# Optimization experiments

Hardware: AMD Instinct MI355X
Metric: run time of the kernel (lower is better)

Reference implementation:

```python
import jax, jax.numpy as jnp
import numpy as np
from functools import partial

T_DEC, T_ENC = 64, 256
B, E, D = 32, 256, 512   # batch, audio_encoder_size(=input_size), decoder_hidden_size
N_MEL = 80               # spectral_size == n_mel_channels


def setup_inputs() -> dict:
    key = jax.random.key(0)
    ks = jax.random.split(key, 9)
    s = 0.02
    return {
        "decoder_inputs": jax.random.normal(ks[0], (T_DEC, B, E), jnp.float32),
        "alignment_inputs": jax.random.normal(ks[1], (T_ENC, B, E), jnp.float32),
        "W_att": jax.random.normal(ks[2], (E, D), jnp.float32) * s,      # LinearNorm(D->E, no bias)
        "W_ih": jax.random.normal(ks[3], (3 * D, 2 * E), jnp.float32) * s,  # GRUCell input weights (r,z,n)
        "W_hh": jax.random.normal(ks[4], (3 * D, D), jnp.float32) * s,      # GRUCell hidden weights
        "W_mel": jax.random.normal(ks[5], (N_MEL, D + E), jnp.float32) * s,
        "b_mel": jax.random.normal(ks[6], (N_MEL,), jnp.float32) * s,
        "W_gate": jax.random.normal(ks[7], (1, D + E), jnp.float32) * s,
        "b_gate": jax.random.normal(ks[8], (1,), jnp.float32) * s,
    }


def _decode_loop(decoder_inputs, alignment_inputs, W_att, W_ih, W_hh, W_mel, b_mel, W_gate, b_gate):
    Bd, Dd = decoder_inputs.shape[1], W_hh.shape[1]

    def step(h, dec_in):
        # --- Attention: per-feature softmax over encoder time, collapsed over features ---
        proj = h @ W_att.T                                  # (B, E)
        scores = alignment_inputs * proj[None]              # (T_enc, B, E)
        w = jax.nn.softmax(scores, axis=0)                  # softmax over encoder time
        tw = w.sum(axis=-1)                                 # (T_enc, B): sum of per-feature weights
        ctx = jnp.einsum('tb,tbe->be', tw, alignment_inputs)  # (B, E)
        # --- GRUCell (bias=False) ---
        x = jnp.concatenate([dec_in, ctx], axis=-1)         # (B, 2E)
        gi = x @ W_ih.T                                     # (B, 3D)
        gh = h @ W_hh.T                                     # (B, 3D)
        ir, iz, inn = jnp.split(gi, 3, axis=-1)
        hr, hz, hn = jnp.split(gh, 3, axis=-1)
        r = jax.nn.sigmoid(ir + hr)
        z = jax.nn.sigmoid(iz + hz)
        n = jnp.tanh(inn + r * hn)
        h_new = (1.0 - z) * n + z * h
        h_new = jax.nn.relu(h_new)                          # relu(dropout(h)), dropout=0
        # --- Output heads ---
        dhac = jnp.concatenate([ctx, h_new], axis=-1)       # (B, E+D)
        mel = dhac @ W_mel.T + b_mel                        # (B, N_MEL)
        gate = dhac @ W_gate.T + b_gate                     # (B, 1)
        return h_new, (mel, gate)

    # prepend zero init frame, drop last frame (teacher forcing, T_dec steps)
    init_frame = jnp.zeros((1,) + decoder_inputs.shape[1:], decoder_inputs.dtype)
    seq = jnp.concatenate([init_frame, decoder_inputs[:-1]], axis=0)
    h0 = jnp.zeros((Bd, Dd), decoder_inputs.dtype)
    _, (mels, gates) = jax.lax.scan(step, h0, seq)
    # parse_decoder_outputs
    n_mel = W_mel.shape[0]
    mel_out = mels.transpose(1, 0, 2).reshape(Bd, -1, n_mel).transpose(0, 2, 1)  # (B, n_mel, T_dec)
    gate_out = gates.transpose(1, 0, 2)                                          # (B, T_dec, 1)
    return mel_out, gate_out


def reference(decoder_inputs, alignment_inputs, W_att, W_ih, W_hh, W_mel, b_mel, W_gate, b_gate):
    return _decode_loop(decoder_inputs, alignment_inputs, W_att, W_ih, W_hh,
                        W_mel, b_mel, W_gate, b_gate)
```

## Files before the change

### kernel.cpp

```cpp
#include <hip/hip_runtime.h>
#include <hip/hip_bf16.h>


#define LOG2E 1.4426950408889634f
#define FLAGS_MAGIC 0x13572468u
#define SMEM_BYTES 138752
#define NBLK 162

typedef __attribute__((ext_vector_type(8))) short bf8;
typedef __attribute__((ext_vector_type(4))) float f32x4;
typedef __attribute__((ext_vector_type(4))) unsigned u32x4;
typedef unsigned long long ull;

#define EX2(x) exp2f(x)
#define MFMA16(a, b, c) __builtin_amdgcn_mfma_f32_16x16x32_bf16(a, b, c, 0, 0, 0)

struct Params {
  const float* dec;
  const float* ali;
  const float* watt;
  const float* wih;
  const float* whh;
  const float* wmel;
  const float* bmel;
  const float* wgate;
  const float* bgate;
  float* out;
  unsigned* bar;
  __hip_bfloat16* wihb;
  __hip_bfloat16* whhb;
  __hip_bfloat16* wmelgb;
  __hip_bfloat16* seqb;
  __hip_bfloat16* hbf;
  __hip_bfloat16* ctxb;
  unsigned* wattp;
};

__device__ __forceinline__ bf8 ldfrag(const __hip_bfloat16* p) { return *(const bf8*)p; }
__device__ __forceinline__ float sigm(float x) { return 1.0f / (1.0f + EX2(-x * LOG2E)); }
__device__ __forceinline__ float tanhfast(float x) {
  x = fminf(fmaxf(x, -15.0f), 15.0f);
  float e = EX2(x * (2.0f * LOG2E));
  return (e - 1.0f) / (e + 1.0f);
}
__device__ __forceinline__ float btof(unsigned v) { return __uint_as_float(v << 16); }
__device__ __forceinline__ unsigned short f2bfbits(float x) {
  __hip_bfloat16 h = __float2bfloat16(x);
  return *(unsigned short*)&h;
}
__device__ __forceinline__ unsigned sysld32(const unsigned* p) {
  return __hip_atomic_load(p, __ATOMIC_RELAXED, __HIP_MEMORY_SCOPE_SYSTEM);
}
__device__ __forceinline__ ull sysld64(const ull* p) {
  return __hip_atomic_load(p, __ATOMIC_RELAXED, __HIP_MEMORY_SCOPE_SYSTEM);
}
__device__ __forceinline__ void sysst32(unsigned* p, unsigned v) {
  __hip_atomic_store(p, v, __ATOMIC_RELAXED, __HIP_MEMORY_SCOPE_SYSTEM);
}
__device__ __forceinline__ void sysst64(ull* p, ull v) {
  __hip_atomic_store(p, v, __ATOMIC_RELAXED, __HIP_MEMORY_SCOPE_SYSTEM);
}
__device__ __forceinline__ void sysld16x4(u32x4* d0, u32x4* d1, u32x4* d2, u32x4* d3,
                                          const void* p0, const void* p1,
                                          const void* p2, const void* p3) {
  u32x4 a, b, c, d;
  asm volatile(
      "global_load_dwordx4 %0, %4, off sc0 sc1\n\t"
      "global_load_dwordx4 %1, %5, off sc0 sc1\n\t"
      "global_load_dwordx4 %2, %6, off sc0 sc1\n\t"
      "global_load_dwordx4 %3, %7, off sc0 sc1\n\t"
      "s_waitcnt vmcnt(0)"
      : "=&v"(a), "=&v"(b), "=&v"(c), "=&v"(d)
      : "v"(p0), "v"(p1), "v"(p2), "v"(p3)
      : "memory");
  *d0 = a; *d1 = b; *d2 = c; *d3 = d;
}
__device__ __forceinline__ void sysld16x8(u32x4* d0, u32x4* d1, u32x4* d2, u32x4* d3,
                                          u32x4* d4, u32x4* d5, u32x4* d6, u32x4* d7,
                                          const void* p0, const void* p1,
                                          const void* p2, const void* p3,
                                          const void* p4, const void* p5,
                                          const void* p6, const void* p7) {
  u32x4 a, b, c, d, e, f, g, h;
  asm volatile(
      "global_load_dwordx4 %0, %8, off sc0 sc1\n\t"
      "global_load_dwordx4 %1, %9, off sc0 sc1\n\t"
      "global_load_dwordx4 %2, %10, off sc0 sc1\n\t"
      "global_load_dwordx4 %3, %11, off sc0 sc1\n\t"
      "global_load_dwordx4 %4, %12, off sc0 sc1\n\t"
      "global_load_dwordx4 %5, %13, off sc0 sc1\n\t"
      "global_load_dwordx4 %6, %14, off sc0 sc1\n\t"
      "global_load_dwordx4 %7, %15, off sc0 sc1\n\t"
      "s_waitcnt vmcnt(0)"
      : "=&v"(a), "=&v"(b), "=&v"(c), "=&v"(d),
        "=&v"(e), "=&v"(f), "=&v"(g), "=&v"(h)
      : "v"(p0), "v"(p1), "v"(p2), "v"(p3),
        "v"(p4), "v"(p5), "v"(p6), "v"(p7)
      : "memory");
  *d0 = a; *d1 = b; *d2 = c; *d3 = d;
  *d4 = e; *d5 = f; *d6 = g; *d7 = h;
}
__device__ __forceinline__ void waitge(unsigned* w, unsigned tgt) {
  while (sysld32(w) < tgt) __builtin_amdgcn_s_sleep(1);
}

__device__ __forceinline__ void p0bar(unsigned* bar) {
  __syncthreads();
  if (threadIdx.x == 0) {
    __builtin_amdgcn_fence(__ATOMIC_RELEASE, "agent");
    __hip_atomic_fetch_add(bar + 16, 1u, __ATOMIC_RELAXED, __HIP_MEMORY_SCOPE_SYSTEM);
    while (sysld32(bar + 16) < (unsigned)NBLK) __builtin_amdgcn_s_sleep(1);
    __builtin_amdgcn_fence(__ATOMIC_ACQUIRE, "agent");
  }
  __syncthreads();
}

__device__ __forceinline__ void p0a_worker(const Params& p, int wid) {
  for (int i = wid; i < 2252800; i += 17408) {
    if (i < 786432) {
      p.wihb[i] = __float2bfloat16(p.wih[i]);
    } else if (i < 1572864) {
      int j = i - 786432;
      p.whhb[j] = __float2bfloat16(p.whh[j]);
    } else if (i < 2097152) {
      int j = i - 1572864;
      int s = j >> 13;
      p.seqb[j] = (s == 0) ? __float2bfloat16(0.0f) : __float2bfloat16(p.dec[j - 8192]);
    } else if (i < 2170880) {
      int j = i - 2097152;
      int r = j / 768, c = j - r * 768;
      float v = (r < 80) ? p.wmel[j] : ((r == 80) ? p.wgate[c] : 0.0f);
      p.wmelgb[j] = __float2bfloat16(v);
    } else if (i < 2236416) {
      int j = i - 2170880;
      int kp = j >> 8, e = j & 255;
      unsigned lo = f2bfbits(p.watt[e * 512 + 2 * kp]);
      unsigned hi = f2bfbits(p.watt[e * 512 + 2 * kp + 1]);
      p.wattp[j] = lo | (hi << 16);
    } else {
      int j = i - 2236416;
      p.hbf[j] = __float2bfloat16(0.0f);
    }
  }
}

__device__ __forceinline__ void stage_h_frag(__hip_bfloat16* hA,
                                             const __hip_bfloat16* hsrc, int tid) {
  const int lm = tid & 15, lq = (tid >> 4) & 3, wq = tid >> 6;
  const int dst_in = (lq * 16 + lm) * 8;
  const int i0 = wq, i1 = 8 + wq, i2 = 16 + wq, i3 = 24 + wq;
  auto soff = [&](int idx) {
    return ((idx >> 4) * 16 + lm) * 512 + (idx & 15) * 32 + lq * 8;
  };
  u32x4 a, b, c, d;
  sysld16x4(&a, &b, &c, &d, hsrc + soff(i0), hsrc + soff(i1), hsrc + soff(i2),
            hsrc + soff(i3));
  u32x4* dst = (u32x4*)hA;
  dst[(i0 * 512 + dst_in) >> 3] = a;
  dst[(i1 * 512 + dst_in) >> 3] = b;
  dst[(i2 * 512 + dst_in) >> 3] = c;
  dst[(i3 * 512 + dst_in) >> 3] = d;
}
__device__ __forceinline__ void stage_c4(__hip_bfloat16* cA,
                                         const __hip_bfloat16* csrc, int tid) {
  const int lm = tid & 15, lq = (tid >> 4) & 3, wq = tid >> 6;
  const int dst_in = (lq * 16 + lm) * 8;
  u32x4* dst = (u32x4*)cA;
  auto soff = [&](int idx) {
    int mt = idx >> 5, kt = idx & 31;
    int bb = mt * 16 + lm;
    int k = kt * 32 + lq * 8;
    return ((k >> 8) * 32 + bb) * 256 + (k & 255);
  };
  const int i0 = wq, i1 = 8 + wq, i2 = 16 + wq, i3 = 24 + wq;
  const int i4 = 32 + wq, i5 = 40 + wq, i6 = 48 + wq, i7 = 56 + wq;
  u32x4 a, b, c, d, e, f, g, h;
  sysld16x8(&a, &b, &c, &d, &e, &f, &g, &h,
            csrc + soff(i0), csrc + soff(i1), csrc + soff(i2), csrc + soff(i3),
            csrc + soff(i4), csrc + soff(i5), csrc + soff(i6), csrc + soff(i7));
  dst[(i0 * 512 + dst_in) >> 3] = a;
  dst[(i1 * 512 + dst_in) >> 3] = b;
  dst[(i2 * 512 + dst_in) >> 3] = c;
  dst[(i3 * 512 + dst_in) >> 3] = d;
  dst[(i4 * 512 + dst_in) >> 3] = e;
  dst[(i5 * 512 + dst_in) >> 3] = f;
  dst[(i6 * 512 + dst_in) >> 3] = g;
  dst[(i7 * 512 + dst_in) >> 3] = h;
}

__global__ void __launch_bounds__(512, 1) rdec_kernel(Params p) {
  const int tid = threadIdx.x;
  const int bid = blockIdx.x;
  extern __shared__ char smem[];
  unsigned* hdone = p.bar + 32;
  unsigned* ctxdone = p.bar + 544;
  unsigned* meldone = p.bar + 2592;

  if (bid == 0) {
    for (int i = 1 + tid; i < 2624; i += 512) sysst32(p.bar + i, 0u);
    __syncthreads();
    if (tid == 0) sysst32(p.bar, FLAGS_MAGIC);
  }

  if (bid < 128) {
    const int b = bid >> 2, q4 = bid & 3, hb = q4 * 32 + b;
    unsigned short* alds = (unsigned short*)smem;
    float* fb = (float*)(smem + 133120);
    float* shh = fb;
    float* p2l = fb + 512;
    float* rzl = fb + 576;
    float* tw = fb + 640;
    float* cp = fb + 896;

    const int el = (tid & 7) | ((tid >> 6) << 3);
    const int kq = (tid >> 3) & 7;
    const int f = tid & 255, th = tid >> 8;

    for (int i = tid; i < 65536; i += 512) {
      int t = i >> 8, ee = i & 255;
      alds[ee * 260 + t] = f2bfbits(p.ali[t * 8192 + b * 256 + ee]);
    }
    if (tid == 0) {
      while (sysld32(p.bar) != FLAGS_MAGIC) __builtin_amdgcn_s_sleep(1);
    }
    p0bar(p.bar);
    unsigned wr[32];
#pragma unroll
    for (int i = 0; i < 32; ++i) wr[i] = p.wattp[(i * 8 + kq) * 256 + q4 * 64 + el];

    for (int s = 0; s < 64; ++s) {
      if (tid < 32) waitge(hdone + tid * 16, (unsigned)s);
      else if (tid < 34) waitge(meldone + (tid - 32) * 16, (s >= 4) ? (unsigned)(s - 3) : 0u);
      __syncthreads();
      if (tid < 128) {
        ull w = sysld64((const ull*)(p.hbf + (s & 3) * 16384 + b * 512) + tid);
        shh[tid * 4 + 0] = btof((unsigned)(w & 0xffff));
        shh[tid * 4 + 1] = btof((unsigned)((w >> 16) & 0xffff));
        shh[tid * 4 + 2] = btof((unsigned)((w >> 32) & 0xffff));
        shh[tid * 4 + 3] = btof((unsigned)((w >> 48) & 0xffff));
      }
      __syncthreads();
      {
        const float2* h2 = (const float2*)shh;
        float a0 = 0.f, a1 = 0.f;
#pragma unroll
        for (int i = 0; i < 32; i += 2) {
          unsigned w0 = wr[i], w1 = wr[i + 1];
          float2 h0 = h2[i * 8 + kq], h1 = h2[(i + 1) * 8 + kq];
          a0 = fmaf(__uint_as_float(w0 << 16), h0.x, a0);
          a0 = fmaf(__uint_as_float(w0 & 0xffff0000u), h0.y, a0);
          a1 = fmaf(__uint_as_float(w1 << 16), h1.x, a1);
          a1 = fmaf(__uint_as_float(w1 & 0xffff0000u), h1.y, a1);
        }
        float pr = a0 + a1;
        pr += __shfl_xor(pr, 8);
        pr += __shfl_xor(pr, 16);
        pr += __shfl_xor(pr, 32);
        const float pp = pr * LOG2E;
        const unsigned short* ap = alds + (q4 * 64 + el) * 260 + kq * 32;
        float z0 = 0.f, z1 = 0.f;
#pragma unroll
        for (int j = 0; j < 8; ++j) {
          ushort4 v = *(const ushort4*)(ap + j * 4);
          z0 += EX2(btof(v.x) * pp) + EX2(btof(v.y) * pp);
          z1 += EX2(btof(v.z) * pp) + EX2(btof(v.w) * pp);
        }
        float zz = z0 + z1;
        zz += __shfl_xor(zz, 8);
        zz += __shfl_xor(zz, 16);
        zz += __shfl_xor(zz, 32);
        if (kq == 0) {
          p2l[el] = pp;
          rzl[el] = 1.0f / zz;
        }
      }
      __syncthreads();
      {
        float t0 = 0.f, t1 = 0.f, t2 = 0.f, t3 = 0.f;
#pragma unroll
        for (int j = 0; j < 8; ++j) {
          const int e2 = kq * 8 + j;
          ushort4 v = *(const ushort4*)(alds + (q4 * 64 + e2) * 260 + el * 4);
          const float ppj = p2l[e2], rr = rzl[e2];
          t0 = fmaf(EX2(btof(v.x) * ppj), rr, t0);
          t1 = fmaf(EX2(btof(v.y) * ppj), rr, t1);
          t2 = fmaf(EX2(btof(v.z) * ppj), rr, t2);
          t3 = fmaf(EX2(btof(v.w) * ppj), rr, t3);
        }
        t0 += __shfl_xor(t0, 8); t0 += __shfl_xor(t0, 16); t0 += __shfl_xor(t0, 32);
        t1 += __shfl_xor(t1, 8); t1 += __shfl_xor(t1, 16); t1 += __shfl_xor(t1, 32);
        t2 += __shfl_xor(t2, 8); t2 += __shfl_xor(t2, 16); t2 += __shfl_xor(t2, 32);
        t3 += __shfl_xor(t3, 8); t3 += __shfl_xor(t3, 16); t3 += __shfl_xor(t3, 32);
        if (kq == 0) *(float4*)(tw + el * 4) = make_float4(t0, t1, t2, t3);
      }
      __syncthreads();
      {
        const unsigned short* ap = alds + f * 260 + th * 128;
        const float4* twv = (const float4*)(tw + th * 128);
        float c0 = 0.f, c1 = 0.f;
#pragma unroll 4
        for (int j = 0; j < 32; ++j) {
          ushort4 v = *(const ushort4*)(ap + j * 4);
          float4 t4 = twv[j];
          c0 += t4.x * btof(v.x) + t4.y * btof(v.y);
          c1 += t4.z * btof(v.z) + t4.w * btof(v.w);
        }
        cp[th * 256 + f] = c0 + c1;
      }
      __syncthreads();
      if (tid < 128) {
        float2 ca = ((const float2*)cp)[tid];
        float2 cb = ((const float2*)(cp + 256))[tid];
        float cv0 = ca.x + cb.x, cv1 = ca.y + cb.y;
        unsigned u = (unsigned)f2bfbits(cv0) | ((unsigned)f2bfbits(cv1) << 16);
        sysst32((unsigned*)(p.ctxb + ((s & 3) * 128 + hb) * 256) + tid, u);
      }
      __syncthreads();
      if (tid == 0) sysst32(ctxdone + hb * 16, (unsigned)(s + 1));
    }
  } else if (bid < 160) {
    const int dt = bid - 128;
    const int wv = tid >> 6;
    const bool act = wv < 6;
    const int l = tid & 63, lm = l & 15, lq = l >> 4;
    const int g = wv % 3, mt = wv / 3;
    const int am = mt * 16 + lm;
    const int brow = g * 512 + dt * 16 + lm;
    __hip_bfloat16* hA = (__hip_bfloat16*)smem;
    __hip_bfloat16* cA = (__hip_bfloat16*)(smem + 32768);
    float* pw = (float*)(smem + 98304);
    unsigned short* h16 = (unsigned short*)(smem + 107008);
    p0a_worker(p, (bid - 128) * 512 + tid);
    if (tid == 0) {
      while (sysld32(p.bar) != FLAGS_MAGIC) __builtin_amdgcn_s_sleep(1);
    }
    p0bar(p.bar);
    bf8 WH[16], WD[8], WC[8];
    if (act) {
#pragma unroll
      for (int kt = 0; kt < 16; ++kt) WH[kt] = ldfrag(p.whhb + brow * 512 + kt * 32 + lq * 8);
#pragma unroll
      for (int kt = 0; kt < 8; ++kt) WD[kt] = ldfrag(p.wihb + brow * 512 + kt * 32 + lq * 8);
#pragma unroll
      for (int kt = 0; kt < 8; ++kt) WC[kt] = ldfrag(p.wihb + brow * 512 + 256 + kt * 32 + lq * 8);
    }
    for (int s = 0; s < 64; ++s) {
      if (tid < 32) waitge(hdone + tid * 16, (unsigned)s);
      else if (tid < 34) waitge(meldone + (tid - 32) * 16, (s >= 4) ? (unsigned)(s - 3) : 0u);
      __syncthreads();
      stage_h_frag(hA, p.hbf + (s & 3) * 16384, tid);
      __syncthreads();
      f32x4 acc = {0.f, 0.f, 0.f, 0.f};
      f32x4 gi = {0.f, 0.f, 0.f, 0.f};
      if (act) {
#pragma unroll
        for (int kt = 0; kt < 16; ++kt) {
          bf8 a = ldfrag(hA + (mt * 16 + kt) * 512 + l * 8);
          acc = MFMA16(a, WH[kt], acc);
        }
        const __hip_bfloat16* seqp = p.seqb + s * 8192;
#pragma unroll
        for (int kt = 0; kt < 8; ++kt) {
          bf8 a = ldfrag(seqp + am * 256 + kt * 32 + lq * 8);
          gi = MFMA16(a, WD[kt], gi);
        }
      }
      if (tid < 128) waitge(ctxdone + tid * 16, (unsigned)(s + 1));
      __syncthreads();
      stage_c4(cA, p.ctxb + (s & 3) * 32768, tid);
      __syncthreads();
      if (act) {
#pragma unroll
        for (int kt = 0; kt < 32; ++kt) {
          bf8 a = ldfrag(cA + (mt * 32 + kt) * 512 + l * 8);
          gi = MFMA16(a, WC[kt & 7], gi);
        }
        if (g < 2) {
#pragma unroll
          for (int r = 0; r < 4; ++r) pw[(wv * 16 + lq * 4 + r) * 17 + lm] = acc[r] + gi[r];
        } else {
#pragma unroll
          for (int r = 0; r < 4; ++r) pw[(wv * 16 + lq * 4 + r) * 17 + lm] = acc[r];
#pragma unroll
          for (int r = 0; r < 4; ++r) pw[((6 + mt) * 16 + lq * 4 + r) * 17 + lm] = gi[r];
        }
      }
      __syncthreads();
      {
        const int bb = tid >> 4, dl = tid & 15;
        const int mtb = bb >> 4, bl = bb & 15;
        float rg = sigm(pw[((mtb * 3 + 0) * 16 + bl) * 17 + dl]);
        float zg = sigm(pw[((mtb * 3 + 1) * 16 + bl) * 17 + dl]);
        float hn = pw[((mtb * 3 + 2) * 16 + bl) * 17 + dl];
        float inn = pw[((6 + mtb) * 16 + bl) * 17 + dl];
        float nn = tanhfast(fmaf(rg, hn, inn));
        const int d = dt * 16 + dl;
        float ho = btof(((unsigned short*)hA)[((bb >> 4) * 16 + (d >> 5)) * 512 +
                                              (((d >> 3) & 3) * 16 + (bb & 15)) * 8 +
                                              (d & 7)]);
        float hnew = fmaxf(0.0f, fmaf(zg, ho - nn, nn));
        h16[bb * 16 + dl] = f2bfbits(hnew);
      }
      __syncthreads();
      if (tid < 256) {
        const int bb2 = tid >> 3, dp = tid & 7;
        unsigned v = (unsigned)h16[bb2 * 16 + dp * 2] |
                     ((unsigned)h16[bb2 * 16 + dp * 2 + 1] << 16);
        sysst32((unsigned*)(p.hbf + ((s + 1) & 3) * 16384) + bb2 * 256 + dt * 8 + dp, v);
      }
      __syncthreads();
      if (tid == 0) sysst32(hdone + dt * 16, (unsigned)(s + 1));
    }
  } else {
    const int mt = bid - 160;
    const int wv = tid >> 6;
    const bool act = wv < 6;
    const int l = tid & 63, lm = l & 15, lq = l >> 4;
    const int nt = wv;
    const int bn = nt * 16 + lm;
    __hip_bfloat16* hA = (__hip_bfloat16*)smem;
    __hip_bfloat16* cA = (__hip_bfloat16*)(smem + 32768);
    p0a_worker(p, (bid - 128) * 512 + tid);
    if (tid == 0) {
      while (sysld32(p.bar) != FLAGS_MAGIC) __builtin_amdgcn_s_sleep(1);
    }
    p0bar(p.bar);
    bf8 WMC[8], WMH[16];
    float bias = 0.f;
    if (act) {
#pragma unroll
      for (int kt = 0; kt < 8; ++kt) WMC[kt] = ldfrag(p.wmelgb + bn * 768 + kt * 32 + lq * 8);
#pragma unroll
      for (int kt = 0; kt < 16; ++kt)
        WMH[kt] = ldfrag(p.wmelgb + bn * 768 + 256 + kt * 32 + lq * 8);
      bias = (bn < 80) ? p.bmel[bn] : ((bn == 80) ? p.bgate[0] : 0.f);
    }
    for (int tau = 0; tau < 64; ++tau) {
      if (tid < 32) waitge(hdone + tid * 16, (unsigned)(tau + 1));
      else if (tid >= 64 && tid < 192) waitge(ctxdone + (tid - 64) * 16, (unsigned)(tau + 1));
      __syncthreads();
      stage_h_frag(hA, p.hbf + ((tau + 1) & 3) * 16384, tid);
      stage_c4(cA, p.ctxb + (tau & 3) * 32768, tid);
      __syncthreads();
      if (act) {
        f32x4 acc = {0.f, 0.f, 0.f, 0.f};
#pragma unroll
        for (int kt = 0; kt < 48; ++kt) {
          bf8 a = (kt < 32) ? ldfrag(cA + (mt * 32 + kt) * 512 + l * 8)
                            : ldfrag(hA + (mt * 16 + (kt - 32)) * 512 + l * 8);
          bf8 bb2 = (kt < 32) ? WMC[kt & 7] : WMH[kt - 32];
          acc = MFMA16(a, bb2, acc);
        }
#pragma unroll
        for (int r = 0; r < 4; ++r) {
          int bb = mt * 16 + lq * 4 + r;
          float v = acc[r] + bias;
          if (bn < 80)
            p.out[bb * 5120 + bn * 64 + tau] = v;
          else if (bn == 80)
            p.out[163840 + bb * 64 + tau] = v;
        }
      }
      __syncthreads();
      if (tid == 0) sysst32(meldone + mt * 16, (unsigned)(tau + 1));
    }
  }
}

extern "C" void kernel_launch(void* const* d_in, const int* in_sizes, int n_in,
                              void* d_out, int out_size, void* d_ws, size_t ws_size,
                              hipStream_t stream) {
  Params P;
  P.dec = (const float*)d_in[0];
  P.ali = (const float*)d_in[1];
  P.watt = (const float*)d_in[2];
  P.wih = (const float*)d_in[3];
  P.whh = (const float*)d_in[4];
  P.wmel = (const float*)d_in[5];
  P.bmel = (const float*)d_in[6];
  P.wgate = (const float*)d_in[7];
  P.bgate = (const float*)d_in[8];
  P.out = (float*)d_out;

  char* w = (char*)d_ws;
  size_t o = 0;
  auto nxt = [&](size_t b) {
    char* r = w + o;
    o += (b + 255) & ~(size_t)255;
    return r;
  };
  P.bar = (unsigned*)nxt(16384);
  P.wihb = (__hip_bfloat16*)nxt(1536 * 512 * 2);
  P.whhb = (__hip_bfloat16*)nxt(1536 * 512 * 2);
  P.wmelgb = (__hip_bfloat16*)nxt(96 * 768 * 2);
  P.seqb = (__hip_bfloat16*)nxt(64 * 32 * 256 * 2);
  P.hbf = (__hip_bfloat16*)nxt(4 * 32 * 512 * 2);
  P.ctxb = (__hip_bfloat16*)nxt(4 * 128 * 256 * 2);
  P.wattp = (unsigned*)nxt(256 * 256 * 4);

  (void)hipFuncSetAttribute((const void*)rdec_kernel,
                            hipFuncAttributeMaxDynamicSharedMemorySize, SMEM_BYTES);

  void* args[] = {&P};
  hipError_t err = hipLaunchCooperativeKernel((void*)rdec_kernel, dim3(NBLK), dim3(512),
                                              args, SMEM_BYTES, stream);
  if (err != hipSuccess) {
    rdec_kernel<<<dim3(NBLK), dim3(512), SMEM_BYTES, stream>>>(P);
  }
}
```

Measured before the change: 822.6 us.

## Fold mel/gate head into GRU blocks and compute context via MFMA

Drops the two dedicated mel/gate blocks and runs the output-head MFMAs on idle waves of the first six GRU blocks, reusing the h and ctx tiles those blocks already stage in shared memory. This removes the meldone back-pressure waits and the extra grid-barrier participants. The attention context reduction becomes an MFMA, with the softmax weights split into high and low bf16 halves to keep precision. The encoder LDS row stride is padded to 264, and the spin-wait loses its sleep so it polls more aggressively, which raises memory-system traffic while blocks wait.

```diff
diff --git a/kernel.cpp b/kernel.cpp
--- a/kernel.cpp
+++ b/kernel.cpp
@@ -4,8 +4,8 @@
 
 #define LOG2E 1.4426950408889634f
 #define FLAGS_MAGIC 0x13572468u
-#define SMEM_BYTES 138752
-#define NBLK 162
+#define SMEM_BYTES 139776
+#define NBLK 160
 
 typedef __attribute__((ext_vector_type(8))) short bf8;
 typedef __attribute__((ext_vector_type(4))) float f32x4;
@@ -101,7 +101,7 @@
   *d4 = e; *d5 = f; *d6 = g; *d7 = h;
 }
 __device__ __forceinline__ void waitge(unsigned* w, unsigned tgt) {
-  while (sysld32(w) < tgt) __builtin_amdgcn_s_sleep(1);
+  while (sysld32(w) < tgt) {}
 }
 
 __device__ __forceinline__ void p0bar(unsigned* bar) {
@@ -116,7 +116,7 @@
 }
 
 __device__ __forceinline__ void p0a_worker(const Params& p, int wid) {
-  for (int i = wid; i < 2252800; i += 17408) {
+  for (int i = wid; i < 2252800; i += 16384) {
     if (i < 786432) {
       p.wihb[i] = __float2bfloat16(p.wih[i]);
     } else if (i < 1572864) {
@@ -194,7 +194,6 @@
   extern __shared__ char smem[];
   unsigned* hdone = p.bar + 32;
   unsigned* ctxdone = p.bar + 544;
-  unsigned* meldone = p.bar + 2592;
 
   if (bid == 0) {
     for (int i = 1 + tid; i < 2624; i += 512) sysst32(p.bar + i, 0u);
@@ -205,20 +204,21 @@
   if (bid < 128) {
     const int b = bid >> 2, q4 = bid & 3, hb = q4 * 32 + b;
     unsigned short* alds = (unsigned short*)smem;
-    float* fb = (float*)(smem + 133120);
+    float* fb = (float*)(smem + 135168);
     float* shh = fb;
     float* p2l = fb + 512;
     float* rzl = fb + 576;
-    float* tw = fb + 640;
-    float* cp = fb + 896;
+    float* ctxf = fb + 640;
+    unsigned short* twb = (unsigned short*)(fb + 896);
 
     const int el = (tid & 7) | ((tid >> 6) << 3);
     const int kq = (tid >> 3) & 7;
-    const int f = tid & 255, th = tid >> 8;
+    const int w = tid >> 6, l = tid & 63;
+    const int lm = l & 15, lq = l >> 4;
 
     for (int i = tid; i < 65536; i += 512) {
       int t = i >> 8, ee = i & 255;
-      alds[ee * 260 + t] = f2bfbits(p.ali[t * 8192 + b * 256 + ee]);
+      alds[ee * 264 + t] = f2bfbits(p.ali[t * 8192 + b * 256 + ee]);
     }
     if (tid == 0) {
       while (sysld32(p.bar) != FLAGS_MAGIC) __builtin_amdgcn_s_sleep(1);
@@ -230,14 +230,13 @@
 
     for (int s = 0; s < 64; ++s) {
       if (tid < 32) waitge(hdone + tid * 16, (unsigned)s);
-      else if (tid < 34) waitge(meldone + (tid - 32) * 16, (s >= 4) ? (unsigned)(s - 3) : 0u);
       __syncthreads();
       if (tid < 128) {
-        ull w = sysld64((const ull*)(p.hbf + (s & 3) * 16384 + b * 512) + tid);
-        shh[tid * 4 + 0] = btof((unsigned)(w & 0xffff));
-        shh[tid * 4 + 1] = btof((unsigned)((w >> 16) & 0xffff));
-        shh[tid * 4 + 2] = btof((unsigned)((w >> 32) & 0xffff));
-        shh[tid * 4 + 3] = btof((unsigned)((w >> 48) & 0xffff));
+        ull wv = sysld64((const ull*)(p.hbf + (s & 3) * 16384 + b * 512) + tid);
+        shh[tid * 4 + 0] = btof((unsigned)(wv & 0xffff));
+        shh[tid * 4 + 1] = btof((unsigned)((wv >> 16) & 0xffff));
+        shh[tid * 4 + 2] = btof((unsigned)((wv >> 32) & 0xffff));
+        shh[tid * 4 + 3] = btof((unsigned)((wv >> 48) & 0xffff));
       }
       __syncthreads();
       {
@@ -257,7 +256,7 @@
         pr += __shfl_xor(pr, 16);
         pr += __shfl_xor(pr, 32);
         const float pp = pr * LOG2E;
-        const unsigned short* ap = alds + (q4 * 64 + el) * 260 + kq * 32;
+        const unsigned short* ap = alds + (q4 * 64 + el) * 264 + kq * 32;
         float z0 = 0.f, z1 = 0.f;
 #pragma unroll
         for (int j = 0; j < 8; ++j) {
@@ -280,7 +279,7 @@
 #pragma unroll
         for (int j = 0; j < 8; ++j) {
           const int e2 = kq * 8 + j;
-          ushort4 v = *(const ushort4*)(alds + (q4 * 64 + e2) * 260 + el * 4);
+          ushort4 v = *(const ushort4*)(alds + (q4 * 64 + e2) * 264 + el * 4);
           const float ppj = p2l[e2], rr = rzl[e2];
           t0 = fmaf(EX2(btof(v.x) * ppj), rr, t0);
           t1 = fmaf(EX2(btof(v.y) * ppj), rr, t1);
@@ -291,34 +290,49 @@
         t1 += __shfl_xor(t1, 8); t1 += __shfl_xor(t1, 16); t1 += __shfl_xor(t1, 32);
         t2 += __shfl_xor(t2, 8); t2 += __shfl_xor(t2, 16); t2 += __shfl_xor(t2, 32);
         t3 += __shfl_xor(t3, 8); t3 += __shfl_xor(t3, 16); t3 += __shfl_xor(t3, 32);
-        if (kq == 0) *(float4*)(tw + el * 4) = make_float4(t0, t1, t2, t3);
+        if (kq == 0) {
+          unsigned short h0 = f2bfbits(t0), h1 = f2bfbits(t1);
+          unsigned short h2c = f2bfbits(t2), h3 = f2bfbits(t3);
+          unsigned short l0 = f2bfbits(t0 - btof(h0)), l1 = f2bfbits(t1 - btof(h1));
+          unsigned short l2 = f2bfbits(t2 - btof(h2c)), l3 = f2bfbits(t3 - btof(h3));
+          *(ull*)(twb + el * 4) =
+              (ull)h0 | ((ull)h1 << 16) | ((ull)h2c << 32) | ((ull)h3 << 48);
+          *(ull*)(twb + 256 + el * 4) =
+              (ull)l0 | ((ull)l1 << 16) | ((ull)l2 << 32) | ((ull)l3 << 48);
+        }
       }
       __syncthreads();
       {
-        const unsigned short* ap = alds + f * 260 + th * 128;
-        const float4* twv = (const float4*)(tw + th * 128);
-        float c0 = 0.f, c1 = 0.f;
-#pragma unroll 4
-        for (int j = 0; j < 32; ++j) {
-          ushort4 v = *(const ushort4*)(ap + j * 4);
-          float4 t4 = twv[j];
-          c0 += t4.x * btof(v.x) + t4.y * btof(v.y);
-          c1 += t4.z * btof(v.z) + t4.w * btof(v.w);
-        }
-        cp[th * 256 + f] = c0 + c1;
+        bf8 tb[16];
+#pragma unroll
+        for (int kt = 0; kt < 16; ++kt)
+          tb[kt] = *(const bf8*)(twb + (kt >> 3) * 256 + (kt & 7) * 32 + lq * 8);
+#pragma unroll
+        for (int half = 0; half < 2; ++half) {
+          const int mt = w * 2 + half;
+          bf8 af[8];
+#pragma unroll
+          for (int kt = 0; kt < 8; ++kt)
+            af[kt] = *(const bf8*)(alds + (mt * 16 + lm) * 264 + kt * 32 + lq * 8);
+          f32x4 acc = {0.f, 0.f, 0.f, 0.f};
+#pragma unroll
+          for (int kt = 0; kt < 16; ++kt) acc = MFMA16(af[kt & 7], tb[kt], acc);
+          if (lm == 0) {
+#pragma unroll
+            for (int r = 0; r < 4; ++r) ctxf[mt * 16 + lq * 4 + r] = acc[r];
+          }
+        }
       }
       __syncthreads();
       if (tid < 128) {
-        float2 ca = ((const float2*)cp)[tid];
-        float2 cb = ((const float2*)(cp + 256))[tid];
-        float cv0 = ca.x + cb.x, cv1 = ca.y + cb.y;
+        float cv0 = ctxf[2 * tid], cv1 = ctxf[2 * tid + 1];
         unsigned u = (unsigned)f2bfbits(cv0) | ((unsigned)f2bfbits(cv1) << 16);
         sysst32((unsigned*)(p.ctxb + ((s & 3) * 128 + hb) * 256) + tid, u);
       }
       __syncthreads();
       if (tid == 0) sysst32(ctxdone + hb * 16, (unsigned)(s + 1));
     }
-  } else if (bid < 160) {
+  } else {
     const int dt = bid - 128;
     const int wv = tid >> 6;
     const bool act = wv < 6;
@@ -344,9 +358,22 @@
 #pragma unroll
       for (int kt = 0; kt < 8; ++kt) WC[kt] = ldfrag(p.wihb + brow * 512 + 256 + kt * 32 + lq * 8);
     }
+    const bool melw = (dt < 6) && (wv >= 6);
+    bf8 WMC[8], WMH[16];
+    float mbias = 0.f;
+    int mmt = 0, bn = 0;
+    if (melw) {
+      mmt = wv - 6;
+      bn = dt * 16 + lm;
+#pragma unroll
+      for (int kt = 0; kt < 8; ++kt) WMC[kt] = ldfrag(p.wmelgb + bn * 768 + kt * 32 + lq * 8);
+#pragma unroll
+      for (int kt = 0; kt < 16; ++kt)
+        WMH[kt] = ldfrag(p.wmelgb + bn * 768 + 256 + kt * 32 + lq * 8);
+      mbias = (bn < 80) ? p.bmel[bn] : ((bn == 80) ? p.bgate[0] : 0.f);
+    }
     for (int s = 0; s < 64; ++s) {
       if (tid < 32) waitge(hdone + tid * 16, (unsigned)s);
-      else if (tid < 34) waitge(meldone + (tid - 32) * 16, (s >= 4) ? (unsigned)(s - 3) : 0u);
       __syncthreads();
       stage_h_frag(hA, p.hbf + (s & 3) * 16384, tid);
       __syncthreads();
@@ -363,6 +390,25 @@
         for (int kt = 0; kt < 8; ++kt) {
           bf8 a = ldfrag(seqp + am * 256 + kt * 32 + lq * 8);
           gi = MFMA16(a, WD[kt], gi);
+        }
+      } else if (melw && s > 0) {
+        const int tau = s - 1;
+        f32x4 macc = {0.f, 0.f, 0.f, 0.f};
+#pragma unroll
+        for (int kt = 0; kt < 48; ++kt) {
+          bf8 a = (kt < 32) ? ldfrag(cA + (mmt * 32 + kt) * 512 + l * 8)
+                            : ldfrag(hA + (mmt * 16 + (kt - 32)) * 512 + l * 8);
+          bf8 bb2 = (kt < 32) ? WMC[kt & 7] : WMH[kt - 32];
+          macc = MFMA16(a, bb2, macc);
+        }
+#pragma unroll
+        for (int r = 0; r < 4; ++r) {
+          int bb = mmt * 16 + lq * 4 + r;
+          float v = macc[r] + mbias;
+          if (bn < 80)
+            p.out[bb * 5120 + bn * 64 + tau] = v;
+          else if (bn == 80)
+            p.out[163840 + bb * 64 + tau] = v;
         }
       }
       if (tid < 128) waitge(ctxdone + tid * 16, (unsigned)(s + 1));
@@ -411,58 +457,30 @@
       __syncthreads();
       if (tid == 0) sysst32(hdone + dt * 16, (unsigned)(s + 1));
     }
-  } else {
-    const int mt = bid - 160;
-    const int wv = tid >> 6;
-    const bool act = wv < 6;
-    const int l = tid & 63, lm = l & 15, lq = l >> 4;
-    const int nt = wv;
-    const int bn = nt * 16 + lm;
-    __hip_bfloat16* hA = (__hip_bfloat16*)smem;
-    __hip_bfloat16* cA = (__hip_bfloat16*)(smem + 32768);
-    p0a_worker(p, (bid - 128) * 512 + tid);
-    if (tid == 0) {
-      while (sysld32(p.bar) != FLAGS_MAGIC) __builtin_amdgcn_s_sleep(1);
-    }
-    p0bar(p.bar);
-    bf8 WMC[8], WMH[16];
-    float bias = 0.f;
-    if (act) {
-#pragma unroll
-      for (int kt = 0; kt < 8; ++kt) WMC[kt] = ldfrag(p.wmelgb + bn * 768 + kt * 32 + lq * 8);
-#pragma unroll
-      for (int kt = 0; kt < 16; ++kt)
-        WMH[kt] = ldfrag(p.wmelgb + bn * 768 + 256 + kt * 32 + lq * 8);
-      bias = (bn < 80) ? p.bmel[bn] : ((bn == 80) ? p.bgate[0] : 0.f);
-    }
-    for (int tau = 0; tau < 64; ++tau) {
-      if (tid < 32) waitge(hdone + tid * 16, (unsigned)(tau + 1));
-      else if (tid >= 64 && tid < 192) waitge(ctxdone + (tid - 64) * 16, (unsigned)(tau + 1));
-      __syncthreads();
-      stage_h_frag(hA, p.hbf + ((tau + 1) & 3) * 16384, tid);
-      stage_c4(cA, p.ctxb + (tau & 3) * 32768, tid);
-      __syncthreads();
-      if (act) {
-        f32x4 acc = {0.f, 0.f, 0.f, 0.f};
+    if (dt < 6) {
+      if (tid < 32) waitge(hdone + tid * 16, 64u);
+      __syncthreads();
+      stage_h_frag(hA, p.hbf + 0, tid);
+      __syncthreads();
+      if (melw) {
+        f32x4 macc = {0.f, 0.f, 0.f, 0.f};
 #pragma unroll
         for (int kt = 0; kt < 48; ++kt) {
-          bf8 a = (kt < 32) ? ldfrag(cA + (mt * 32 + kt) * 512 + l * 8)
-                            : ldfrag(hA + (mt * 16 + (kt - 32)) * 512 + l * 8);
+          bf8 a = (kt < 32) ? ldfrag(cA + (mmt * 32 + kt) * 512 + l * 8)
+                            : ldfrag(hA + (mmt * 16 + (kt - 32)) * 512 + l * 8);
           bf8 bb2 = (kt < 32) ? WMC[kt & 7] : WMH[kt - 32];
-          acc = MFMA16(a, bb2, acc);
+          macc = MFMA16(a, bb2, macc);
         }
 #pragma unroll
         for (int r = 0; r < 4; ++r) {
-          int bb = mt * 16 + lq * 4 + r;
-          float v = acc[r] + bias;
+          int bb = mmt * 16 + lq * 4 + r;
+          float v = macc[r] + mbias;
           if (bn < 80)
-            p.out[bb * 5120 + bn * 64 + tau] = v;
+            p.out[bb * 5120 + bn * 64 + 63] = v;
           else if (bn == 80)
-            p.out[163840 + bb * 64 + tau] = v;
-        }
-      }
-      __syncthreads();
-      if (tid == 0) sysst32(meldone + mt * 16, (unsigned)(tau + 1));
+            p.out[163840 + bb * 64 + 63] = v;
+        }
+      }
     }
   }
 }
```

New measurement: 856.6 us. +4.1%, slower.

## Publish ctx/h from one wavefront with drained stores, move flag polling to idle waves

Applied to the files above, without the earlier changes.

The ctx and h publication is narrowed to a single wavefront that issues wider system-scope stores, waits for them to drain, and then raises the done flag. This removes a block-wide __syncthreads between the data store and the flag store. The flag-polling lanes move to higher-numbered waves so they do not sit in the wavefront doing the stores or the MFMA work. Ordering now relies on the in-wave vmcnt drain instead of a block barrier, which is subtle for cross-block visibility, and the next iteration's barrier still serializes later work.

```diff
diff --git a/kernel.cpp b/kernel.cpp
--- a/kernel.cpp
+++ b/kernel.cpp
@@ -59,6 +59,14 @@
 }
 __device__ __forceinline__ void sysst64(ull* p, ull v) {
   __hip_atomic_store(p, v, __ATOMIC_RELAXED, __HIP_MEMORY_SCOPE_SYSTEM);
+}
+__device__ __forceinline__ void sysst8_drain(void* dst, ull v) {
+  asm volatile("global_store_dwordx2 %0, %1, off sc0 sc1\n\ts_waitcnt vmcnt(0)"
+               :: "v"(dst), "v"(v) : "memory");
+}
+__device__ __forceinline__ void sysst16_drain(void* dst, u32x4 v) {
+  asm volatile("global_store_dwordx4 %0, %1, off sc0 sc1\n\ts_waitcnt vmcnt(0)"
+               :: "v"(dst), "v"(v) : "memory");
 }
 __device__ __forceinline__ void sysld16x4(u32x4* d0, u32x4* d1, u32x4* d2, u32x4* d3,
                                           const void* p0, const void* p1,
@@ -229,8 +237,9 @@
     for (int i = 0; i < 32; ++i) wr[i] = p.wattp[(i * 8 + kq) * 256 + q4 * 64 + el];
 
     for (int s = 0; s < 64; ++s) {
-      if (tid < 32) waitge(hdone + tid * 16, (unsigned)s);
-      else if (tid < 34) waitge(meldone + (tid - 32) * 16, (s >= 4) ? (unsigned)(s - 3) : 0u);
+      if (tid >= 128 && tid < 160) waitge(hdone + (tid - 128) * 16, (unsigned)s);
+      else if (tid >= 160 && tid < 162)
+        waitge(meldone + (tid - 160) * 16, (s >= 4) ? (unsigned)(s - 3) : 0u);
       __syncthreads();
       if (tid < 128) {
         ull w = sysld64((const ull*)(p.hbf + (s & 3) * 16384 + b * 512) + tid);
@@ -308,15 +317,17 @@
         cp[th * 256 + f] = c0 + c1;
       }
       __syncthreads();
-      if (tid < 128) {
-        float2 ca = ((const float2*)cp)[tid];
-        float2 cb = ((const float2*)(cp + 256))[tid];
-        float cv0 = ca.x + cb.x, cv1 = ca.y + cb.y;
-        unsigned u = (unsigned)f2bfbits(cv0) | ((unsigned)f2bfbits(cv1) << 16);
-        sysst32((unsigned*)(p.ctxb + ((s & 3) * 128 + hb) * 256) + tid, u);
-      }
-      __syncthreads();
-      if (tid == 0) sysst32(ctxdone + hb * 16, (unsigned)(s + 1));
+      if (tid < 64) {
+        float4 ca = *(const float4*)(cp + 4 * tid);
+        float4 cb = *(const float4*)(cp + 256 + 4 * tid);
+        unsigned u0 = (unsigned)f2bfbits(ca.x + cb.x) |
+                      ((unsigned)f2bfbits(ca.y + cb.y) << 16);
+        unsigned u1 = (unsigned)f2bfbits(ca.z + cb.z) |
+                      ((unsigned)f2bfbits(ca.w + cb.w) << 16);
+        unsigned* dst = (unsigned*)(p.ctxb + ((s & 3) * 128 + hb) * 256) + 2 * tid;
+        sysst8_drain(dst, (ull)u0 | ((ull)u1 << 32));
+        if (tid == 0) sysst32(ctxdone + hb * 16, (unsigned)(s + 1));
+      }
     }
   } else if (bid < 160) {
     const int dt = bid - 128;
@@ -345,8 +356,9 @@
       for (int kt = 0; kt < 8; ++kt) WC[kt] = ldfrag(p.wihb + brow * 512 + 256 + kt * 32 + lq * 8);
     }
     for (int s = 0; s < 64; ++s) {
-      if (tid < 32) waitge(hdone + tid * 16, (unsigned)s);
-      else if (tid < 34) waitge(meldone + (tid - 32) * 16, (s >= 4) ? (unsigned)(s - 3) : 0u);
+      if (tid >= 384 && tid < 416) waitge(hdone + (tid - 384) * 16, (unsigned)s);
+      else if (tid >= 416 && tid < 418)
+        waitge(meldone + (tid - 416) * 16, (s >= 4) ? (unsigned)(s - 3) : 0u);
       __syncthreads();
       stage_h_frag(hA, p.hbf + (s & 3) * 16384, tid);
       __syncthreads();
@@ -365,7 +377,7 @@
           gi = MFMA16(a, WD[kt], gi);
         }
       }
-      if (tid < 128) waitge(ctxdone + tid * 16, (unsigned)(s + 1));
+      if (tid >= 384) waitge(ctxdone + (tid - 384) * 16, (unsigned)(s + 1));
       __syncthreads();
       stage_c4(cA, p.ctxb + (s & 3) * 32768, tid);
       __syncthreads();
@@ -402,14 +414,13 @@
         h16[bb * 16 + dl] = f2bfbits(hnew);
       }
       __syncthreads();
-      if (tid < 256) {
-        const int bb2 = tid >> 3, dp = tid & 7;
-        unsigned v = (unsigned)h16[bb2 * 16 + dp * 2] |
-                     ((unsigned)h16[bb2 * 16 + dp * 2 + 1] << 16);
-        sysst32((unsigned*)(p.hbf + ((s + 1) & 3) * 16384) + bb2 * 256 + dt * 8 + dp, v);
-      }
-      __syncthreads();
-      if (tid == 0) sysst32(hdone + dt * 16, (unsigned)(s + 1));
+      if (tid < 64) {
+        u32x4 hv = *(const u32x4*)(h16 + 8 * tid);
+        unsigned* dst = (unsigned*)(p.hbf + ((s + 1) & 3) * 16384) +
+                        (tid >> 1) * 256 + dt * 8 + (tid & 1) * 4;
+        sysst16_drain(dst, hv);
+        if (tid == 0) sysst32(hdone + dt * 16, (unsigned)(s + 1));
+      }
     }
   } else {
     const int mt = bid - 160;
```

Result: slower. 886.5 us (+7.8%).

## Replace flag-based step barriers with sentinel-polled, non-reused data buffers

Applied to the files above, without the earlier changes.

Removes the per-step done counters and waits. Consumers now poll the h and ctx data directly until no sentinel value remains. The ring buffers of depth 4 are replaced with fully unrolled buffers (65 steps for h, 64 for ctx) that are pre-filled with a sentinel, so producers never wait on consumers (the meldone back-pressure is gone). This cuts one flag round-trip and several __syncthreads per step, at the cost of more workspace memory and a sentinel fill at startup, plus a risk that the sentinel fill races with early producer writes or that a bf16 pair legitimately equals the sentinel.

```diff
diff --git a/kernel.cpp b/kernel.cpp
--- a/kernel.cpp
+++ b/kernel.cpp
@@ -4,6 +4,7 @@
 
 #define LOG2E 1.4426950408889634f
 #define FLAGS_MAGIC 0x13572468u
+#define SENT 0x7FFF7FFFu
 #define SMEM_BYTES 138752
 #define NBLK 162
 
@@ -55,9 +56,6 @@
   return __hip_atomic_load(p, __ATOMIC_RELAXED, __HIP_MEMORY_SCOPE_SYSTEM);
 }
 __device__ __forceinline__ void sysst32(unsigned* p, unsigned v) {
-  __hip_atomic_store(p, v, __ATOMIC_RELAXED, __HIP_MEMORY_SCOPE_SYSTEM);
-}
-__device__ __forceinline__ void sysst64(ull* p, ull v) {
   __hip_atomic_store(p, v, __ATOMIC_RELAXED, __HIP_MEMORY_SCOPE_SYSTEM);
 }
 __device__ __forceinline__ void sysld16x4(u32x4* d0, u32x4* d1, u32x4* d2, u32x4* d3,
@@ -100,8 +98,8 @@
   *d0 = a; *d1 = b; *d2 = c; *d3 = d;
   *d4 = e; *d5 = f; *d6 = g; *d7 = h;
 }
-__device__ __forceinline__ void waitge(unsigned* w, unsigned tgt) {
-  while (sysld32(w) < tgt) __builtin_amdgcn_s_sleep(1);
+__device__ __forceinline__ bool clean4(u32x4 v) {
+  return v[0] != SENT && v[1] != SENT && v[2] != SENT && v[3] != SENT;
 }
 
 __device__ __forceinline__ void p0bar(unsigned* bar) {
@@ -144,7 +142,7 @@
   }
 }
 
-__device__ __forceinline__ void stage_h_frag(__hip_bfloat16* hA,
+__device__ __forceinline__ void stage_h_poll(__hip_bfloat16* hA,
                                              const __hip_bfloat16* hsrc, int tid) {
   const int lm = tid & 15, lq = (tid >> 4) & 3, wq = tid >> 6;
   const int dst_in = (lq * 16 + lm) * 8;
@@ -153,16 +151,20 @@
     return ((idx >> 4) * 16 + lm) * 512 + (idx & 15) * 32 + lq * 8;
   };
   u32x4 a, b, c, d;
-  sysld16x4(&a, &b, &c, &d, hsrc + soff(i0), hsrc + soff(i1), hsrc + soff(i2),
-            hsrc + soff(i3));
+  for (;;) {
+    sysld16x4(&a, &b, &c, &d, hsrc + soff(i0), hsrc + soff(i1), hsrc + soff(i2),
+              hsrc + soff(i3));
+    if (clean4(a) && clean4(b) && clean4(c) && clean4(d)) break;
+    __builtin_amdgcn_s_sleep(1);
+  }
   u32x4* dst = (u32x4*)hA;
   dst[(i0 * 512 + dst_in) >> 3] = a;
   dst[(i1 * 512 + dst_in) >> 3] = b;
   dst[(i2 * 512 + dst_in) >> 3] = c;
   dst[(i3 * 512 + dst_in) >> 3] = d;
 }
-__device__ __forceinline__ void stage_c4(__hip_bfloat16* cA,
-                                         const __hip_bfloat16* csrc, int tid) {
+__device__ __forceinline__ void stage_c4_poll(__hip_bfloat16* cA,
+                                              const __hip_bfloat16* csrc, int tid) {
   const int lm = tid & 15, lq = (tid >> 4) & 3, wq = tid >> 6;
   const int dst_in = (lq * 16 + lm) * 8;
   u32x4* dst = (u32x4*)cA;
@@ -175,9 +177,14 @@
   const int i0 = wq, i1 = 8 + wq, i2 = 16 + wq, i3 = 24 + wq;
   const int i4 = 32 + wq, i5 = 40 + wq, i6 = 48 + wq, i7 = 56 + wq;
   u32x4 a, b, c, d, e, f, g, h;
-  sysld16x8(&a, &b, &c, &d, &e, &f, &g, &h,
-            csrc + soff(i0), csrc + soff(i1), csrc + soff(i2), csrc + soff(i3),
-            csrc + soff(i4), csrc + soff(i5), csrc + soff(i6), csrc + soff(i7));
+  for (;;) {
+    sysld16x8(&a, &b, &c, &d, &e, &f, &g, &h,
+              csrc + soff(i0), csrc + soff(i1), csrc + soff(i2), csrc + soff(i3),
+              csrc + soff(i4), csrc + soff(i5), csrc + soff(i6), csrc + soff(i7));
+    if (clean4(a) && clean4(b) && clean4(c) && clean4(d) &&
+        clean4(e) && clean4(f) && clean4(g) && clean4(h)) break;
+    __builtin_amdgcn_s_sleep(1);
+  }
   dst[(i0 * 512 + dst_in) >> 3] = a;
   dst[(i1 * 512 + dst_in) >> 3] = b;
   dst[(i2 * 512 + dst_in) >> 3] = c;
@@ -192,9 +199,6 @@
   const int tid = threadIdx.x;
   const int bid = blockIdx.x;
   extern __shared__ char smem[];
-  unsigned* hdone = p.bar + 32;
-  unsigned* ctxdone = p.bar + 544;
-  unsigned* meldone = p.bar + 2592;
 
   if (bid == 0) {
     for (int i = 1 + tid; i < 2624; i += 512) sysst32(p.bar + i, 0u);
@@ -216,6 +220,12 @@
     const int kq = (tid >> 3) & 7;
     const int f = tid & 255, th = tid >> 8;
 
+    {
+      unsigned* hb32 = (unsigned*)p.hbf;
+      unsigned* cb32 = (unsigned*)p.ctxb;
+      for (int i = bid * 512 + tid; i < 524288; i += 65536) hb32[8192 + i] = SENT;
+      for (int i = bid * 512 + tid; i < 1048576; i += 65536) cb32[i] = SENT;
+    }
     for (int i = tid; i < 65536; i += 512) {
       int t = i >> 8, ee = i & 255;
       alds[ee * 260 + t] = f2bfbits(p.ali[t * 8192 + b * 256 + ee]);
@@ -229,11 +239,14 @@
     for (int i = 0; i < 32; ++i) wr[i] = p.wattp[(i * 8 + kq) * 256 + q4 * 64 + el];
 
     for (int s = 0; s < 64; ++s) {
-      if (tid < 32) waitge(hdone + tid * 16, (unsigned)s);
-      else if (tid < 34) waitge(meldone + (tid - 32) * 16, (s >= 4) ? (unsigned)(s - 3) : 0u);
-      __syncthreads();
       if (tid < 128) {
-        ull w = sysld64((const ull*)(p.hbf + (s & 3) * 16384 + b * 512) + tid);
+        const ull* hsrc = (const ull*)(p.hbf + s * 16384 + b * 512) + tid;
+        ull w;
+        for (;;) {
+          w = sysld64(hsrc);
+          if ((unsigned)w != SENT && (unsigned)(w >> 32) != SENT) break;
+          __builtin_amdgcn_s_sleep(1);
+        }
         shh[tid * 4 + 0] = btof((unsigned)(w & 0xffff));
         shh[tid * 4 + 1] = btof((unsigned)((w >> 16) & 0xffff));
         shh[tid * 4 + 2] = btof((unsigned)((w >> 32) & 0xffff));
@@ -313,10 +326,9 @@
         float2 cb = ((const float2*)(cp + 256))[tid];
         float cv0 = ca.x + cb.x, cv1 = ca.y + cb.y;
         unsigned u = (unsigned)f2bfbits(cv0) | ((unsigned)f2bfbits(cv1) << 16);
-        sysst32((unsigned*)(p.ctxb + ((s & 3) * 128 + hb) * 256) + tid, u);
-      }
-      __syncthreads();
-      if (tid == 0) sysst32(ctxdone + hb * 16, (unsigned)(s + 1));
+        sysst32((unsigned*)(p.ctxb + (s * 128 + hb) * 256) + tid, u);
+      }
+      __syncthreads();
     }
   } else if (bid < 160) {
     const int dt = bid - 128;
@@ -345,10 +357,7 @@
       for (int kt = 0; kt < 8; ++kt) WC[kt] = ldfrag(p.wihb + brow * 512 + 256 + kt * 32 + lq * 8);
     }
     for (int s = 0; s < 64; ++s) {
-      if (tid < 32) waitge(hdone + tid * 16, (unsigned)s);
-      else if (tid < 34) waitge(meldone + (tid - 32) * 16, (s >= 4) ? (unsigned)(s - 3) : 0u);
-      __syncthreads();
-      stage_h_frag(hA, p.hbf + (s & 3) * 16384, tid);
+      stage_h_poll(hA, p.hbf + s * 16384, tid);
       __syncthreads();
       f32x4 acc = {0.f, 0.f, 0.f, 0.f};
       f32x4 gi = {0.f, 0.f, 0.f, 0.f};
@@ -365,9 +374,7 @@
           gi = MFMA16(a, WD[kt], gi);
         }
       }
-      if (tid < 128) waitge(ctxdone + tid * 16, (unsigned)(s + 1));
-      __syncthreads();
-      stage_c4(cA, p.ctxb + (s & 3) * 32768, tid);
+      stage_c4_poll(cA, p.ctxb + s * 32768, tid);
       __syncthreads();
       if (act) {
 #pragma unroll
@@ -406,10 +413,9 @@
         const int bb2 = tid >> 3, dp = tid & 7;
         unsigned v = (unsigned)h16[bb2 * 16 + dp * 2] |
                      ((unsigned)h16[bb2 * 16 + dp * 2 + 1] << 16);
-        sysst32((unsigned*)(p.hbf + ((s + 1) & 3) * 16384) + bb2 * 256 + dt * 8 + dp, v);
-      }
-      __syncthreads();
-      if (tid == 0) sysst32(hdone + dt * 16, (unsigned)(s + 1));
+        sysst32((unsigned*)(p.hbf + (s + 1) * 16384) + bb2 * 256 + dt * 8 + dp, v);
+      }
+      __syncthreads();
     }
   } else {
     const int mt = bid - 160;
@@ -436,11 +442,8 @@
       bias = (bn < 80) ? p.bmel[bn] : ((bn == 80) ? p.bgate[0] : 0.f);
     }
     for (int tau = 0; tau < 64; ++tau) {
-      if (tid < 32) waitge(hdone + tid * 16, (unsigned)(tau + 1));
-      else if (tid >= 64 && tid < 192) waitge(ctxdone + (tid - 64) * 16, (unsigned)(tau + 1));
-      __syncthreads();
-      stage_h_frag(hA, p.hbf + ((tau + 1) & 3) * 16384, tid);
-      stage_c4(cA, p.ctxb + (tau & 3) * 32768, tid);
+      stage_h_poll(hA, p.hbf + (tau + 1) * 16384, tid);
+      stage_c4_poll(cA, p.ctxb + tau * 32768, tid);
       __syncthreads();
       if (act) {
         f32x4 acc = {0.f, 0.f, 0.f, 0.f};
@@ -462,7 +465,6 @@
         }
       }
       __syncthreads();
-      if (tid == 0) sysst32(meldone + mt * 16, (unsigned)(tau + 1));
     }
   }
 }
@@ -494,8 +496,8 @@
   P.whhb = (__hip_bfloat16*)nxt(1536 * 512 * 2);
   P.wmelgb = (__hip_bfloat16*)nxt(96 * 768 * 2);
   P.seqb = (__hip_bfloat16*)nxt(64 * 32 * 256 * 2);
-  P.hbf = (__hip_bfloat16*)nxt(4 * 32 * 512 * 2);
-  P.ctxb = (__hip_bfloat16*)nxt(4 * 128 * 256 * 2);
+  P.hbf = (__hip_bfloat16*)nxt(65 * 32 * 512 * 2);
+  P.ctxb = (__hip_bfloat16*)nxt(64 * 128 * 256 * 2);
   P.wattp = (unsigned*)nxt(256 * 256 * 4);
 
   (void)hipFuncSetAttribute((const void*)rdec_kernel,
```

After: 822.5 us. Within noise of the previous version (-0.0%).
